# Performance work log

Measured on AMD Instinct MI355X. Metric: run time of the kernel, lower is better.

## Reference

```python
import jax, jax.numpy as jnp
import numpy as np

B_NODES, C_FEAT, I_DIM = 2048, 128, 9  # nodes, num_features, coupling irreps dim (0e+1o+2e)
M_OUT = {'s': 1, 'p': 3, 'd': 5}       # output irrep dims for 0e, 1o, 2e
K_PATHS = {'s': [1, 2, 5], 'p': [1, 3, 8], 'd': [1, 4, 10]}  # CG path counts per correlation


def setup_inputs() -> dict:
    key = jax.random.key(0)
    ks = jax.random.split(key, 32)
    inp = {'A': jax.random.normal(ks[0], (B_NODES, C_FEAT, I_DIM), dtype=jnp.float32)}
    idx = 1
    for t in ('s', 'p', 'd'):
        m = M_OUT[t]
        for nu in (1, 2, 3):
            k = K_PATHS[t][nu - 1]
            inp[f'U_{t}{nu}'] = jax.random.normal(ks[idx], (m,) + (I_DIM,) * nu + (k,), dtype=jnp.float32)
            idx += 1
            inp[f'w_{t}{nu}'] = jax.random.normal(ks[idx], (k, C_FEAT), dtype=jnp.float32) * 0.1
            idx += 1
    return inp


def _contract(A, U1, U2, U3, w1, w2, w3):
    # body-order 3 init: U3 [m,i,i,i,k], w3 [k,c], A [b,c,i] -> B [b,c,m,i,i]
    B = jnp.einsum('...ik,kc,bci->bc...', U3, w3, A)
    for U, w in ((U2, w2), (U1, w1)):
        C = jnp.einsum('...k,kc->c...', U, w) + B   # broadcast residual over batch
        B = jnp.einsum('bc...i,bci->bc...', C, A)   # contract one i axis per step
    return B  # [b, c, m]


def reference(A, U_s1, U_s2, U_s3, U_p1, U_p2, U_p3, U_d1, U_d2, U_d3,
              w_s1, w_s2, w_s3, w_p1, w_p2, w_p3, w_d1, w_d2, w_d3):
    B_s = _contract(A, U_s1, U_s2, U_s3, w_s1, w_s2, w_s3)
    B_p = _contract(A, U_p1, U_p2, U_p3, w_p1, w_p2, w_p3)
    B_d = _contract(A, U_d1, U_d2, U_d3, w_d1, w_d2, w_d3)
    return jnp.concatenate([B_s, B_p, B_d], axis=-1)  # [b, c, 1+3+5]
```

## Files before the change

kernel.cpp:

```cpp
#include <hip/hip_runtime.h>
#include <hip/hip_bf16.h>

#define CFEAT 128
#define NODES 2048
#define NM    219
#define NSTEP 7

typedef __attribute__((ext_vector_type(8))) short short8;
typedef __attribute__((ext_vector_type(4))) float f32x4;
typedef __attribute__((ext_vector_type(4))) unsigned int uint4v;

#define OFF3 262144
#define OFF2 (OFF3 + 9*165*16)
#define OFF1 (OFF2 + 9*45*4)

__device__ __forceinline__ short f2bf(float x) {
    union { __hip_bfloat16 b; short s; } cv;
    cv.b = __float2bfloat16(x);
    return cv.s;
}

struct MIdx { int deg, i, j, l; };
__host__ __device__ constexpr MIdx decode_c(int idx) {
    if (idx < 9) return {1, idx, 0, 0};
    int t = idx - 9;
    for (int i = 0; i < 9; ++i)
        for (int j = i; j < 9; ++j) {
            int cnt = 10 - j;
            if (t < cnt) {
                if (t == 0) return {2, i, j, 0};
                return {3, i, j, j + t - 1};
            }
            t -= cnt;
        }
    return {0, 0, 0, 0};
}
__host__ __device__ constexpr int h2c(int n) { return n * (n + 1) / 2; }
__host__ __device__ constexpr int g3c(int n) { return n * (n + 1) * (n + 2) / 6; }
__host__ __device__ constexpr int tri3c(int i, int j, int l) {
    return (165 - g3c(9 - i)) + (h2c(9 - i) - h2c(9 - j)) + (l - j);
}
__host__ __device__ constexpr int pair2c(int i, int j) {
    return (45 - h2c(9 - i)) + (j - i);
}

struct MTbl { int v[224]; };
__host__ __device__ constexpr MTbl gen_tbl() {
    MTbl t{};
    for (int k = 0; k < 224; ++k) {
        if (k < NM) {
            MIdx d = decode_c(k);
            int sub = (d.deg == 1) ? d.i : (d.deg == 2) ? pair2c(d.i, d.j)
                                                        : tri3c(d.i, d.j, d.l);
            t.v[k] = d.deg | (sub << 4);
        } else t.v[k] = 0;
    }
    return t;
}
__device__ constexpr MTbl MONO_TBL = gen_tbl();

template<int K>
__device__ __forceinline__ float mono_val_t(const float a[9]) {
    if constexpr (K >= NM) return 0.f;
    else {
        constexpr MIdx d = decode_c(K);
        if constexpr (d.deg == 1) return a[d.i];
        else if constexpr (d.deg == 2) return a[d.i] * a[d.j];
        else return a[d.i] * a[d.j] * a[d.l];
    }
}

template<int KB, int E2>
__device__ __forceinline__ unsigned pack2(const float a[9]) {
    union { struct { short lo, hi; } p; unsigned u; } cv;
    cv.p.lo = f2bf(mono_val_t<KB + 2 * E2>(a));
    cv.p.hi = f2bf(mono_val_t<KB + 2 * E2 + 1>(a));
    return cv.u;
}
template<int KB>
__device__ __forceinline__ uint4v build_granule(const float a[9]) {
    return uint4v{pack2<KB,0>(a), pack2<KB,1>(a), pack2<KB,2>(a), pack2<KB,3>(a)};
}

__global__ __launch_bounds__(256) void symcon_p1(
    const float* __restrict__ Us1, const float* __restrict__ Us2, const float* __restrict__ Us3,
    const float* __restrict__ Up1, const float* __restrict__ Up2, const float* __restrict__ Up3,
    const float* __restrict__ Ud1, const float* __restrict__ Ud2, const float* __restrict__ Ud3,
    float* __restrict__ ws_f)
{
    const int mg = blockIdx.x;
    const int y  = blockIdx.y;
    const int t  = threadIdx.x;

    const float *U1, *U2, *U3; int K2, K3, ml;
    if (mg == 0)     { U1 = Us1; U2 = Us2; U3 = Us3; K2 = 2; K3 = 5;  ml = 0; }
    else if (mg < 4) { U1 = Up1; U2 = Up2; U3 = Up3; K2 = 3; K3 = 8;  ml = mg - 1; }
    else             { U1 = Ud1; U2 = Ud2; U3 = Ud3; K2 = 4; K3 = 10; ml = mg - 4; }

    if (y < 11) {
        if (t >= 240) return;
        const int tri = y * 15 + (t >> 4);
        const int k   = t & 15;
        if (k >= K3) return;
        int i = 0, j = 0, l = 0, r = tri;
        bool done = false;
        for (i = 0; i < 9 && !done; ++i)
            for (j = i; j < 9; ++j) {
                int cnt = 9 - j;
                if (r < cnt) { l = j + r; done = true; break; }
                r -= cnt;
            }
        --i;
        const int e0=(i*9+j)*9+l, e1=(i*9+l)*9+j, e2=(j*9+i)*9+l,
                  e3=(j*9+l)*9+i, e4=(l*9+i)*9+j, e5=(l*9+j)*9+i;
        const float* B3 = U3 + (size_t)ml * 729 * K3 + k;
        float v = B3[(size_t)e0 * K3];
        if (e1 != e0)                                     v += B3[(size_t)e1 * K3];
        if (e2 != e0 && e2 != e1)                         v += B3[(size_t)e2 * K3];
        if (e3 != e0 && e3 != e1 && e3 != e2)             v += B3[(size_t)e3 * K3];
        if (e4 != e0 && e4 != e1 && e4 != e2 && e4 != e3) v += B3[(size_t)e4 * K3];
        if (e5 != e0 && e5 != e1 && e5 != e2 && e5 != e3 && e5 != e4)
                                                          v += B3[(size_t)e5 * K3];
        ws_f[OFF3 + (mg * 165 + tri) * 16 + k] = v;
    } else {
        if (t < 180) {
            int pr = t >> 2, k = t & 3;
            if (k >= K2) return;
            int i = 0, j = 0, r = pr;
            for (i = 0; i < 9; ++i) {
                int cnt = 9 - i;
                if (r < cnt) { j = i + r; break; }
                r -= cnt;
            }
            float v = U2[((size_t)(ml * 9 + i) * 9 + j) * K2 + k];
            if (i != j) v += U2[((size_t)(ml * 9 + j) * 9 + i) * K2 + k];
            ws_f[OFF2 + (mg * 45 + pr) * 4 + k] = v;
        } else if (t < 189) {
            const int i = t - 180;
            ws_f[OFF1 + mg * 9 + i] = U1[ml * 9 + i];
        }
    }
}

__global__ __launch_bounds__(256) void symcon_p2(
    const float* __restrict__ ws_f,
    const float* __restrict__ ws1, const float* __restrict__ ws2, const float* __restrict__ ws3,
    const float* __restrict__ wp1, const float* __restrict__ wp2, const float* __restrict__ wp3,
    const float* __restrict__ wd1, const float* __restrict__ wd2, const float* __restrict__ wd3,
    short* __restrict__ Wf)
{
    const int c = blockIdx.x, s = blockIdx.y >> 1;
    const int slot = ((blockIdx.y & 1) << 8) | threadIdx.x;
    const int lane = slot >> 3, e = slot & 7;
    const int k = s * 32 + ((lane >> 4) * 8) + e;
    const int m = lane & 15;
    float v = 0.f;
    if (k < NM && m < 9) {
        const int pk  = MONO_TBL.v[k];
        const int deg = pk & 15, sub = pk >> 4;
        const float *w1, *w2, *w3; int K2, K3;
        if (m == 0)     { w1 = ws1; w2 = ws2; w3 = ws3; K2 = 2; K3 = 5;  }
        else if (m < 4) { w1 = wp1; w2 = wp2; w3 = wp3; K2 = 3; K3 = 8;  }
        else            { w1 = wd1; w2 = wd2; w3 = wd3; K2 = 4; K3 = 10; }
        if (deg == 1) {
            v = ws_f[OFF1 + m * 9 + sub] * w1[c];
        } else if (deg == 2) {
            const float* u = ws_f + OFF2 + (m * 45 + sub) * 4;
            for (int kk = 0; kk < K2; ++kk) v = fmaf(u[kk], w2[kk * CFEAT + c], v);
        } else {
            const float* u = ws_f + OFF3 + (m * 165 + sub) * 16;
            for (int kk = 0; kk < K3; ++kk) v = fmaf(u[kk], w3[kk * CFEAT + c], v);
        }
    }
    Wf[(((size_t)c * NSTEP + s) * 64 + lane) * 8 + e] = f2bf(v);
}

template<int S>
__device__ __forceinline__ void do_step(const float a[9], char* wrbase, const char* rdbase,
                                        const short8 bfrag[NSTEP], f32x4 acc[4])
{
    const uint4v g0 = build_granule<S * 32 +  0>(a);
    const uint4v g1 = build_granule<S * 32 +  8>(a);
    const uint4v g2 = build_granule<S * 32 + 16>(a);
    const uint4v g3 = build_granule<S * 32 + 24>(a);
    *(uint4v*)(wrbase       ) = g0;
    *(uint4v*)(wrbase + 1024) = g1;
    *(uint4v*)(wrbase + 2048) = g2;
    *(uint4v*)(wrbase + 3072) = g3;
    #pragma unroll
    for (int t = 0; t < 4; ++t) {
        short8 af = *(const short8*)(rdbase + t * 256);
        acc[t] = __builtin_amdgcn_mfma_f32_16x16x32_bf16(af, bfrag[S], acc[t], 0, 0, 0);
    }
}

#define SROW 148
__global__ __launch_bounds__(1024, 1) void symcon_hot(
    const float* __restrict__ A, const short* __restrict__ Wf, float* __restrict__ out)
{
    const int tid = threadIdx.x;
    const int w = tid >> 6, l = tid & 63;
    const int p = l & 15, q = l >> 4;
    const int c0 = blockIdx.x * 16;
    const int nb = blockIdx.y * 64;

    __shared__ float sA[64 * SROW];
    __shared__ __align__(16) char phiAll[16 * 4096];

    const short8* Wc = (const short8*)Wf + (size_t)(c0 + w) * NSTEP * 64;
    short8 bfrag[NSTEP];
    #pragma unroll
    for (int s = 0; s < NSTEP; ++s) bfrag[s] = Wc[s * 64 + l];

    const float* Ap = A + ((size_t)(nb + l) * CFEAT + (c0 + w)) * 9;
    float a[9];
    #pragma unroll
    for (int x = 0; x < 9; ++x) a[x] = Ap[x];

    char* const phiW   = phiAll + w * 4096;
    char* const wrbase = phiW + l * 16;
    const char* const rdbase = phiW + q * 1024 + p * 16;

    f32x4 acc[4];
    #pragma unroll
    for (int t = 0; t < 4; ++t) acc[t] = f32x4{0.f, 0.f, 0.f, 0.f};

    do_step<0>(a, wrbase, rdbase, bfrag, acc);
    do_step<1>(a, wrbase, rdbase, bfrag, acc);
    do_step<2>(a, wrbase, rdbase, bfrag, acc);
    do_step<3>(a, wrbase, rdbase, bfrag, acc);
    do_step<4>(a, wrbase, rdbase, bfrag, acc);
    do_step<5>(a, wrbase, rdbase, bfrag, acc);
    do_step<6>(a, wrbase, rdbase, bfrag, acc);

    if (p < 9) {
        #pragma unroll
        for (int t = 0; t < 4; ++t)
            #pragma unroll
            for (int r = 0; r < 4; ++r)
                sA[(t * 16 + q * 4 + r) * SROW + w * 9 + p] = acc[t][r];
    }
    __syncthreads();

    const size_t gbase = (size_t)nb * (CFEAT * 9) + (size_t)c0 * 9;
    #pragma unroll
    for (int e = tid; e < 64 * 36; e += 1024) {
        const int n = e / 36, f = e - n * 36;
        const float* src = &sA[n * SROW + f * 4];
        const float4 v{src[0], src[1], src[2], src[3]};
        *(float4*)(out + gbase + (size_t)n * (CFEAT * 9) + f * 4) = v;
    }
}

extern "C" void kernel_launch(void* const* d_in, const int* in_sizes, int n_in,
                              void* d_out, int out_size, void* d_ws, size_t ws_size,
                              hipStream_t stream)
{
    const float* A   = (const float*)d_in[0];
    const float* Us1 = (const float*)d_in[1];  const float* ws1 = (const float*)d_in[2];
    const float* Us2 = (const float*)d_in[3];  const float* ws2 = (const float*)d_in[4];
    const float* Us3 = (const float*)d_in[5];  const float* ws3 = (const float*)d_in[6];
    const float* Up1 = (const float*)d_in[7];  const float* wp1 = (const float*)d_in[8];
    const float* Up2 = (const float*)d_in[9];  const float* wp2 = (const float*)d_in[10];
    const float* Up3 = (const float*)d_in[11]; const float* wp3 = (const float*)d_in[12];
    const float* Ud1 = (const float*)d_in[13]; const float* wd1 = (const float*)d_in[14];
    const float* Ud2 = (const float*)d_in[15]; const float* wd2 = (const float*)d_in[16];
    const float* Ud3 = (const float*)d_in[17]; const float* wd3 = (const float*)d_in[18];
    float* out  = (float*)d_out;
    float* ws_f = (float*)d_ws;
    short* Wf   = (short*)d_ws;

    symcon_p1<<<dim3(9, 12), 256, 0, stream>>>(
        Us1, Us2, Us3, Up1, Up2, Up3, Ud1, Ud2, Ud3, ws_f);

    symcon_p2<<<dim3(CFEAT, NSTEP * 2), 256, 0, stream>>>(
        ws_f, ws1, ws2, ws3, wp1, wp2, wp3, wd1, wd2, wd3, Wf);

    symcon_hot<<<dim3(CFEAT / 16, NODES / 64), 1024, 0, stream>>>(A, Wf, out);
}
```

Measured before the change: 26.54 us.

## Fuse weight-symmetrization and channel-mixing prep kernels into one launch

```diff
diff --git a/kernel.cpp b/kernel.cpp
--- a/kernel.cpp
+++ b/kernel.cpp
@@ -9,10 +9,6 @@
 typedef __attribute__((ext_vector_type(8))) short short8;
 typedef __attribute__((ext_vector_type(4))) float f32x4;
 typedef __attribute__((ext_vector_type(4))) unsigned int uint4v;
-
-#define OFF3 262144
-#define OFF2 (OFF3 + 9*165*16)
-#define OFF1 (OFF2 + 9*45*4)
 
 __device__ __forceinline__ short f2bf(float x) {
     union { __hip_bfloat16 b; short s; } cv;
@@ -82,97 +78,123 @@
     return uint4v{pack2<KB,0>(a), pack2<KB,1>(a), pack2<KB,2>(a), pack2<KB,3>(a)};
 }
 
-__global__ __launch_bounds__(256) void symcon_p1(
-    const float* __restrict__ Us1, const float* __restrict__ Us2, const float* __restrict__ Us3,
-    const float* __restrict__ Up1, const float* __restrict__ Up2, const float* __restrict__ Up3,
-    const float* __restrict__ Ud1, const float* __restrict__ Ud2, const float* __restrict__ Ud3,
-    float* __restrict__ ws_f)
+__global__ __launch_bounds__(1024) void symcon_prep(
+    const float* __restrict__ Us1, const float* __restrict__ ws1,
+    const float* __restrict__ Us2, const float* __restrict__ ws2,
+    const float* __restrict__ Us3, const float* __restrict__ ws3,
+    const float* __restrict__ Up1, const float* __restrict__ wp1,
+    const float* __restrict__ Up2, const float* __restrict__ wp2,
+    const float* __restrict__ Up3, const float* __restrict__ wp3,
+    const float* __restrict__ Ud1, const float* __restrict__ wd1,
+    const float* __restrict__ Ud2, const float* __restrict__ wd2,
+    const float* __restrict__ Ud3, const float* __restrict__ wd3,
+    short* __restrict__ Wf)
 {
     const int mg = blockIdx.x;
-    const int y  = blockIdx.y;
     const int t  = threadIdx.x;
 
-    const float *U1, *U2, *U3; int K2, K3, ml;
-    if (mg == 0)     { U1 = Us1; U2 = Us2; U3 = Us3; K2 = 2; K3 = 5;  ml = 0; }
-    else if (mg < 4) { U1 = Up1; U2 = Up2; U3 = Up3; K2 = 3; K3 = 8;  ml = mg - 1; }
-    else             { U1 = Ud1; U2 = Ud2; U3 = Ud3; K2 = 4; K3 = 10; ml = mg - 4; }
-
-    if (y < 11) {
-        if (t >= 240) return;
-        const int tri = y * 15 + (t >> 4);
-        const int k   = t & 15;
-        if (k >= K3) return;
-        int i = 0, j = 0, l = 0, r = tri;
-        bool done = false;
-        for (i = 0; i < 9 && !done; ++i)
-            for (j = i; j < 9; ++j) {
-                int cnt = 9 - j;
-                if (r < cnt) { l = j + r; done = true; break; }
-                r -= cnt;
-            }
-        --i;
-        const int e0=(i*9+j)*9+l, e1=(i*9+l)*9+j, e2=(j*9+i)*9+l,
-                  e3=(j*9+l)*9+i, e4=(l*9+i)*9+j, e5=(l*9+j)*9+i;
-        const float* B3 = U3 + (size_t)ml * 729 * K3 + k;
-        float v = B3[(size_t)e0 * K3];
-        if (e1 != e0)                                     v += B3[(size_t)e1 * K3];
-        if (e2 != e0 && e2 != e1)                         v += B3[(size_t)e2 * K3];
-        if (e3 != e0 && e3 != e1 && e3 != e2)             v += B3[(size_t)e3 * K3];
-        if (e4 != e0 && e4 != e1 && e4 != e2 && e4 != e3) v += B3[(size_t)e4 * K3];
-        if (e5 != e0 && e5 != e1 && e5 != e2 && e5 != e3 && e5 != e4)
-                                                          v += B3[(size_t)e5 * K3];
-        ws_f[OFF3 + (mg * 165 + tri) * 16 + k] = v;
+    __shared__ float U3s[165 * 16];
+    __shared__ float U2s[45 * 4];
+    __shared__ float U1s[16];
+
+    const float *U1, *U2, *U3, *w1, *w2, *w3; int K2, K3, ml;
+    if (mg == 0) {
+        U1 = Us1; U2 = Us2; U3 = Us3; w1 = ws1; w2 = ws2; w3 = ws3;
+        K2 = 2; K3 = 5;  ml = 0;
+    } else if (mg < 4) {
+        U1 = Up1; U2 = Up2; U3 = Up3; w1 = wp1; w2 = wp2; w3 = wp3;
+        K2 = 3; K3 = 8;  ml = mg - 1;
     } else {
-        if (t < 180) {
-            int pr = t >> 2, k = t & 3;
-            if (k >= K2) return;
+        U1 = Ud1; U2 = Ud2; U3 = Ud3; w1 = wd1; w2 = wd2; w3 = wd3;
+        K2 = 4; K3 = 10; ml = mg - 4;
+    }
+
+    for (int e = t; e < 165 * 16; e += 1024) {
+        const int tri = e >> 4, k = e & 15;
+        float v = 0.f;
+        if (k < K3) {
+            int i = 0, j = 0, l = 0, r = tri;
+            bool done = false;
+            for (i = 0; i < 9 && !done; ++i)
+                for (j = i; j < 9; ++j) {
+                    int cnt = 9 - j;
+                    if (r < cnt) { l = j + r; done = true; break; }
+                    r -= cnt;
+                }
+            --i;
+            const int e0=(i*9+j)*9+l, e1=(i*9+l)*9+j, e2=(j*9+i)*9+l,
+                      e3=(j*9+l)*9+i, e4=(l*9+i)*9+j, e5=(l*9+j)*9+i;
+            const float* B3 = U3 + (size_t)ml * 729 * K3 + k;
+            v = B3[(size_t)e0 * K3];
+            if (e1 != e0)                                     v += B3[(size_t)e1 * K3];
+            if (e2 != e0 && e2 != e1)                         v += B3[(size_t)e2 * K3];
+            if (e3 != e0 && e3 != e1 && e3 != e2)             v += B3[(size_t)e3 * K3];
+            if (e4 != e0 && e4 != e1 && e4 != e2 && e4 != e3) v += B3[(size_t)e4 * K3];
+            if (e5 != e0 && e5 != e1 && e5 != e2 && e5 != e3 && e5 != e4)
+                                                              v += B3[(size_t)e5 * K3];
+        }
+        U3s[e] = v;
+    }
+    if (t < 180) {
+        const int pr = t >> 2, k = t & 3;
+        float v = 0.f;
+        if (k < K2) {
             int i = 0, j = 0, r = pr;
             for (i = 0; i < 9; ++i) {
                 int cnt = 9 - i;
                 if (r < cnt) { j = i + r; break; }
                 r -= cnt;
             }
-            float v = U2[((size_t)(ml * 9 + i) * 9 + j) * K2 + k];
+            v = U2[((size_t)(ml * 9 + i) * 9 + j) * K2 + k];
             if (i != j) v += U2[((size_t)(ml * 9 + j) * 9 + i) * K2 + k];
-            ws_f[OFF2 + (mg * 45 + pr) * 4 + k] = v;
-        } else if (t < 189) {
-            const int i = t - 180;
-            ws_f[OFF1 + mg * 9 + i] = U1[ml * 9 + i];
-        }
-    }
-}
-
-__global__ __launch_bounds__(256) void symcon_p2(
-    const float* __restrict__ ws_f,
-    const float* __restrict__ ws1, const float* __restrict__ ws2, const float* __restrict__ ws3,
-    const float* __restrict__ wp1, const float* __restrict__ wp2, const float* __restrict__ wp3,
-    const float* __restrict__ wd1, const float* __restrict__ wd2, const float* __restrict__ wd3,
-    short* __restrict__ Wf)
-{
-    const int c = blockIdx.x, s = blockIdx.y >> 1;
-    const int slot = ((blockIdx.y & 1) << 8) | threadIdx.x;
-    const int lane = slot >> 3, e = slot & 7;
-    const int k = s * 32 + ((lane >> 4) * 8) + e;
-    const int m = lane & 15;
-    float v = 0.f;
-    if (k < NM && m < 9) {
-        const int pk  = MONO_TBL.v[k];
-        const int deg = pk & 15, sub = pk >> 4;
-        const float *w1, *w2, *w3; int K2, K3;
-        if (m == 0)     { w1 = ws1; w2 = ws2; w3 = ws3; K2 = 2; K3 = 5;  }
-        else if (m < 4) { w1 = wp1; w2 = wp2; w3 = wp3; K2 = 3; K3 = 8;  }
-        else            { w1 = wd1; w2 = wd2; w3 = wd3; K2 = 4; K3 = 10; }
-        if (deg == 1) {
-            v = ws_f[OFF1 + m * 9 + sub] * w1[c];
-        } else if (deg == 2) {
-            const float* u = ws_f + OFF2 + (m * 45 + sub) * 4;
-            for (int kk = 0; kk < K2; ++kk) v = fmaf(u[kk], w2[kk * CFEAT + c], v);
-        } else {
-            const float* u = ws_f + OFF3 + (m * 165 + sub) * 16;
-            for (int kk = 0; kk < K3; ++kk) v = fmaf(u[kk], w3[kk * CFEAT + c], v);
-        }
-    }
-    Wf[(((size_t)c * NSTEP + s) * 64 + lane) * 8 + e] = f2bf(v);
+        }
+        U2s[t] = v;
+    } else if (t < 189) {
+        U1s[t - 180] = U1[ml * 9 + (t - 180)];
+    }
+    __syncthreads();
+
+    const int c = t >> 3;
+
+    float wr3[10], wr2[4], wr1;
+    #pragma unroll
+    for (int kk = 0; kk < 10; ++kk) wr3[kk] = (kk < K3) ? w3[kk * CFEAT + c] : 0.f;
+    #pragma unroll
+    for (int kk = 0; kk < 4; ++kk)  wr2[kk] = (kk < K2) ? w2[kk * CFEAT + c] : 0.f;
+    wr1 = w1[c];
+
+    for (int ch = t & 7; ch < 28; ch += 8) {
+        const int s = ch >> 2, kg = ch & 3;
+        short8 pk8;
+        #pragma unroll
+        for (int e = 0; e < 8; ++e) {
+            const int k = s * 32 + kg * 8 + e;
+            const int pk = MONO_TBL.v[k];
+            const int deg = pk & 15, sub = pk >> 4;
+            float v = 0.f;
+            if (deg == 1) {
+                v = U1s[sub] * wr1;
+            } else if (deg == 2) {
+                #pragma unroll
+                for (int kk = 0; kk < 4; ++kk)
+                    v = fmaf(U2s[sub * 4 + kk], wr2[kk], v);
+            } else if (deg == 3) {
+                #pragma unroll
+                for (int kk = 0; kk < 10; ++kk)
+                    v = fmaf(U3s[sub * 16 + kk], wr3[kk], v);
+            }
+            pk8[e] = f2bf(v);
+        }
+        *(short8*)(Wf + (((size_t)c * NSTEP + s) * 64 + (kg * 16 + mg)) * 8) = pk8;
+    }
+
+    if (mg < 7) {
+        const short8 z{};
+        for (int ch = t & 7; ch < 28; ch += 8) {
+            const int s = ch >> 2, kg = ch & 3;
+            *(short8*)(Wf + (((size_t)c * NSTEP + s) * 64 + (kg * 16 + 9 + mg)) * 8) = z;
+        }
+    }
 }
 
 template<int S>
@@ -266,15 +288,12 @@
     const float* Ud1 = (const float*)d_in[13]; const float* wd1 = (const float*)d_in[14];
     const float* Ud2 = (const float*)d_in[15]; const float* wd2 = (const float*)d_in[16];
     const float* Ud3 = (const float*)d_in[17]; const float* wd3 = (const float*)d_in[18];
-    float* out  = (float*)d_out;
-    float* ws_f = (float*)d_ws;
-    short* Wf   = (short*)d_ws;
-
-    symcon_p1<<<dim3(9, 12), 256, 0, stream>>>(
-        Us1, Us2, Us3, Up1, Up2, Up3, Ud1, Ud2, Ud3, ws_f);
-
-    symcon_p2<<<dim3(CFEAT, NSTEP * 2), 256, 0, stream>>>(
-        ws_f, ws1, ws2, ws3, wp1, wp2, wp3, wd1, wd2, wd3, Wf);
+    float* out = (float*)d_out;
+    short* Wf  = (short*)d_ws;
+
+    symcon_prep<<<9, 1024, 0, stream>>>(
+        Us1, ws1, Us2, ws2, Us3, ws3, Up1, wp1, Up2, wp2, Up3, wp3,
+        Ud1, wd1, Ud2, wd2, Ud3, wd3, Wf);
 
     symcon_hot<<<dim3(CFEAT / 16, NODES / 64), 1024, 0, stream>>>(A, Wf, out);
 }
```

After: 38.11 us. 43.6% more time.
